# Performance work log

Measured on AMD Instinct MI355X. Metric: run time of the kernel, lower is better.

## Reference

```python
import jax, jax.numpy as jnp
import numpy as np

H = 256          # hidden_size
L = 2            # num_layers
K = 4            # khops
R = 128          # relation_num
N_NODES = 20000
N_EDGES = 160000
N_LG_EDGES = 640000


def setup_inputs() -> dict:
    key = jax.random.key(0)
    ks = iter(jax.random.split(key, 40))
    def nrm(shape, s=1.0):
        return jax.random.normal(next(ks), shape, dtype=jnp.float32) * s
    w = 1.0 / float(np.sqrt(H))
    return {
        "x": nrm((N_NODES, H)),
        "edge_feat": jax.random.randint(next(ks), (N_EDGES,), 0, R),
        "edge_index_g": jax.random.randint(next(ks), (2, N_EDGES), 0, N_NODES),
        "edge_index_lg": jax.random.randint(next(ks), (2, N_LG_EDGES), 0, N_EDGES),
        "rel_embed": nrm((R, H)),
        # per-layer, per-core (0=node update, 1=edge update) parameter stacks
        "w_self": nrm((L, 2, H, H), w), "b_self": jnp.zeros((L, 2, H), jnp.float32),
        "w_khop": nrm((L, 2, K, H, H), w), "b_khop": jnp.zeros((L, 2, K, H), jnp.float32),
        "w_fuse": nrm((L, 2, H, H), w), "b_fuse": jnp.zeros((L, 2, H), jnp.float32),
        "w_ff1": nrm((L, 2, H, 4 * H), w), "b_ff1": jnp.zeros((L, 2, 4 * H), jnp.float32),
        "w_ff2": nrm((L, 2, 4 * H, H), 1.0 / float(np.sqrt(4 * H))), "b_ff2": jnp.zeros((L, 2, H), jnp.float32),
        "ln1_g": jnp.ones((L, 2, H), jnp.float32), "ln1_b": jnp.zeros((L, 2, H), jnp.float32),
        "ln2_g": jnp.ones((L, 2, H), jnp.float32), "ln2_b": jnp.zeros((L, 2, H), jnp.float32),
    }


def _layernorm(x, g, b, eps=1e-5):
    m = jnp.mean(x, axis=-1, keepdims=True)
    v = jnp.var(x, axis=-1, keepdims=True)
    return (x - m) * jax.lax.rsqrt(v + eps) * g + b


def _core(p, src, dst, x, fused):
    """LGNNCore.forward (eval mode, dropout never applied in core)."""
    (ws, bs, wk, bk, wf, bf, w1, b1, w2, b2, g1, c1, g2, c2) = p
    n = x.shape[0]
    prev = x @ ws + bs
    # k-hop copy_src + sum aggregation, each hop gets its own linear
    z = x
    kh = jnp.zeros_like(prev)
    for i in range(wk.shape[0]):
        z = jax.ops.segment_sum(z[src], dst, num_segments=n)
        kh = kh + z @ wk[i] + bk[i]
    edge = fused @ wf + bf
    out = jax.nn.gelu(prev + kh + edge, approximate=False)
    out = _layernorm(x + out, g1, c1)
    ffn = jax.nn.gelu(out @ w1 + b1, approximate=False) @ w2 + b2
    return _layernorm(out + ffn, g2, c2)


def reference(x, edge_feat, edge_index_g, edge_index_lg, rel_embed,
              w_self, b_self, w_khop, b_khop, w_fuse, b_fuse,
              w_ff1, b_ff1, w_ff2, b_ff2, ln1_g, ln1_b, ln2_g, ln2_b):
    lg_x = rel_embed[edge_feat]                       # [n_edges, H]
    src_g, dst_g = edge_index_g[0], edge_index_g[1]
    src_l, dst_l = edge_index_lg[0], edge_index_lg[1]
    n_nodes = x.shape[0]
    for l in range(w_self.shape[0]):
        def pick(c):
            return (w_self[l, c], b_self[l, c], w_khop[l, c], b_khop[l, c],
                    w_fuse[l, c], b_fuse[l, c], w_ff1[l, c], b_ff1[l, c],
                    w_ff2[l, c], b_ff2[l, c], ln1_g[l, c], ln1_b[l, c],
                    ln2_g[l, c], ln2_b[l, c])
        # pmpd @ lg_x : scatter each edge feature to both of its endpoints
        fused_nodes = (jax.ops.segment_sum(lg_x, src_g, num_segments=n_nodes)
                       + jax.ops.segment_sum(lg_x, dst_g, num_segments=n_nodes))
        # pmpd^T @ x : gather both endpoint node features per edge
        fused_edges = x[src_g] + x[dst_g]
        new_x = _core(pick(0), src_g, dst_g, x, fused_nodes)
        new_lg_x = _core(pick(1), src_l, dst_l, lg_x, fused_edges)
        x, lg_x = new_x, new_lg_x
    return x, lg_x
```

## Files before the change

### kernel.cpp

```cpp
#include <hip/hip_runtime.h>

typedef __bf16 bf16;
typedef __attribute__((ext_vector_type(8))) __bf16 bf16x8;
typedef __attribute__((ext_vector_type(4))) __bf16 bf16x4;
typedef __attribute__((ext_vector_type(4))) float f32x4;

#define HD 256
#define GEMM_GELU 2

__device__ __forceinline__ float gelu_f(float x) {
  return 0.5f * x * (1.0f + erff(x * 0.70710678118654752440f));
}

__device__ __forceinline__ void gload_lds16(const void* g, void* l) {
  __builtin_amdgcn_global_load_lds(
      (const __attribute__((address_space(1))) unsigned int*)g,
      (__attribute__((address_space(3))) unsigned int*)l, 16, 0, 0);
}

__global__ __launch_bounds__(256) void gemm_k(
    const bf16* __restrict__ A, const bf16* __restrict__ Wt,
    const float* __restrict__ bias, bf16* __restrict__ C,
    int M, int Kd, int lda, int ldc, int flags)
{
  __shared__ __align__(16) bf16 sA[128 * 32];
  __shared__ __align__(16) bf16 sB[128 * 32];
  const int t = threadIdx.x;
  const int lane = t & 63, w = t >> 6;
  const int n0 = blockIdx.x * 128, m0 = blockIdx.y * 128;
  const int wr = w >> 1, wc = w & 1;
  const int lm = lane & 15, quad = lane >> 4;

  const int srow = t >> 2;
  const int scolb = (t & 3) * 16;
  const bool full = (m0 + 128 <= M);

  const char* a0 = (const char*)(A + (size_t)(m0 + srow) * lda) + scolb;
  const char* a1 = (const char*)(A + (size_t)(m0 + srow + 64) * lda) + scolb;
  const char* b0 = (const char*)(Wt + (size_t)(n0 + srow) * Kd) + scolb;
  const char* b1 = (const char*)(Wt + (size_t)(n0 + srow + 64) * Kd) + scolb;
  bf16* lA0 = sA + w * 512;
  bf16* lA1 = sA + 2048 + w * 512;
  bf16* lB0 = sB + w * 512;
  bf16* lB1 = sB + 2048 + w * 512;

  f32x4 acc[4][4];
#pragma unroll
  for (int i = 0; i < 4; i++)
#pragma unroll
    for (int j = 0; j < 4; j++)
#pragma unroll
      for (int r = 0; r < 4; r++) acc[i][j][r] = 0.f;

  for (int kb = 0; kb < Kd; kb += 32) {
    size_t ko = (size_t)kb * 2;
    if (full) {
      gload_lds16(a0 + ko, lA0);
      gload_lds16(a1 + ko, lA1);
    } else {
#pragma unroll
      for (int c = 0; c < 2; c++) {
        int row = srow + c * 64;
        int gr = m0 + row;
        bf16x8 va;
#pragma unroll
        for (int q = 0; q < 8; q++) va[q] = (bf16)0.f;
        if (gr < M) va = *(const bf16x8*)((const char*)(A + (size_t)gr * lda) + ko + scolb);
        *(bf16x8*)(sA + row * 32 + (scolb >> 1)) = va;
      }
    }
    gload_lds16(b0 + ko, lB0);
    gload_lds16(b1 + ko, lB1);
    __syncthreads();
    bf16x8 af[4], bv[4];
#pragma unroll
    for (int i = 0; i < 4; i++) af[i] = *(const bf16x8*)(sA + (wr * 64 + i * 16 + lm) * 32 + quad * 8);
#pragma unroll
    for (int j = 0; j < 4; j++) bv[j] = *(const bf16x8*)(sB + (wc * 64 + j * 16 + lm) * 32 + quad * 8);
#pragma unroll
    for (int i = 0; i < 4; i++)
#pragma unroll
      for (int j = 0; j < 4; j++)
        acc[i][j] = __builtin_amdgcn_mfma_f32_16x16x32_bf16(af[i], bv[j], acc[i][j], 0, 0, 0);
    __syncthreads();
  }
#pragma unroll
  for (int i = 0; i < 4; i++) {
#pragma unroll
    for (int r = 0; r < 4; r++) {
      int gr = m0 + wr * 64 + i * 16 + quad * 4 + r;
      if (gr < M) {
#pragma unroll
        for (int j = 0; j < 4; j++) {
          int gc = n0 + wc * 64 + j * 16 + lm;
          float v = acc[i][j][r] + bias[gc];
          if (flags & GEMM_GELU) v = gelu_f(v);
          C[(size_t)gr * ldc + gc] = (bf16)v;
        }
      }
    }
  }
}

__global__ __launch_bounds__(256) void segsum_k(
    const int* __restrict__ offs, const int* __restrict__ cols,
    const bf16* __restrict__ in, int ldin, bf16* __restrict__ out, int ldout, int nseg)
{
  int wid = threadIdx.x >> 6, lane = threadIdx.x & 63;
  int seg = blockIdx.x * 4 + wid;
  if (seg >= nseg) return;
  int b = offs[seg], e = offs[seg + 1];
  float a0 = 0.f, a1 = 0.f, a2 = 0.f, a3 = 0.f;
  for (int i = b; i < e; i++) {
    int c = cols[i];
    bf16x4 v = *(const bf16x4*)(in + (size_t)c * ldin + lane * 4);
    a0 += (float)v.x; a1 += (float)v.y; a2 += (float)v.z; a3 += (float)v.w;
  }
  bf16x4 o = {(bf16)a0, (bf16)a1, (bf16)a2, (bf16)a3};
  *(bf16x4*)(out + (size_t)seg * ldout + lane * 4) = o;
}

__global__ __launch_bounds__(256) void ln_k(
    const bf16* __restrict__ X, int ldx, const bf16* __restrict__ A,
    const float* __restrict__ gam, const float* __restrict__ bet,
    bf16* __restrict__ outb, float* __restrict__ outf, int M, int apply_gelu)
{
  int wid = threadIdx.x >> 6, lane = threadIdx.x & 63;
  int row = blockIdx.x * 4 + wid;
  if (row >= M) return;
  size_t xbase = (size_t)row * ldx + lane * 4;
  size_t abase = (size_t)row * HD + lane * 4;
  bf16x4 xv = *(const bf16x4*)(X + xbase);
  bf16x4 av = *(const bf16x4*)(A + abase);
  float s0, s1, s2, s3;
  if (apply_gelu) {
    s0 = (float)xv.x + gelu_f((float)av.x);
    s1 = (float)xv.y + gelu_f((float)av.y);
    s2 = (float)xv.z + gelu_f((float)av.z);
    s3 = (float)xv.w + gelu_f((float)av.w);
  } else {
    s0 = (float)xv.x + (float)av.x;
    s1 = (float)xv.y + (float)av.y;
    s2 = (float)xv.z + (float)av.z;
    s3 = (float)xv.w + (float)av.w;
  }
  float sum = s0 + s1 + s2 + s3;
#pragma unroll
  for (int o = 32; o; o >>= 1) sum += __shfl_xor(sum, o, 64);
  float mean = sum * (1.0f / 256.0f);
  float d0 = s0 - mean, d1 = s1 - mean, d2 = s2 - mean, d3 = s3 - mean;
  float vs = d0 * d0 + d1 * d1 + d2 * d2 + d3 * d3;
#pragma unroll
  for (int o = 32; o; o >>= 1) vs += __shfl_xor(vs, o, 64);
  float rstd = rsqrtf(vs * (1.0f / 256.0f) + 1e-5f);
  float4 g = *(const float4*)(gam + lane * 4);
  float4 bb = *(const float4*)(bet + lane * 4);
  float y0 = d0 * rstd * g.x + bb.x;
  float y1 = d1 * rstd * g.y + bb.y;
  float y2 = d2 * rstd * g.z + bb.z;
  float y3 = d3 * rstd * g.w + bb.w;
  if (outb) {
    bf16x4 o = {(bf16)y0, (bf16)y1, (bf16)y2, (bf16)y3};
    *(bf16x4*)(outb + xbase) = o;
  }
  if (outf) {
    float4 o = {y0, y1, y2, y3};
    *(float4*)(outf + abase) = o;
  }
}

__global__ __launch_bounds__(256) void gather_rel_k(
    const int* __restrict__ feat, const float* __restrict__ rel,
    bf16* __restrict__ out, int ldout, int NE)
{
  int wid = threadIdx.x >> 6, lane = threadIdx.x & 63;
  int e = blockIdx.x * 4 + wid;
  if (e >= NE) return;
  int f = feat[e];
  float4 v = *(const float4*)(rel + (size_t)f * HD + lane * 4);
  bf16x4 o = {(bf16)v.x, (bf16)v.y, (bf16)v.z, (bf16)v.w};
  *(bf16x4*)(out + (size_t)e * ldout + lane * 4) = o;
}

__global__ __launch_bounds__(256) void gather2_k(
    const int* __restrict__ src, const int* __restrict__ dst,
    const bf16* __restrict__ x, int ldx, bf16* __restrict__ out, int ldout, int NE)
{
  int wid = threadIdx.x >> 6, lane = threadIdx.x & 63;
  int e = blockIdx.x * 4 + wid;
  if (e >= NE) return;
  int s = src[e], d = dst[e];
  bf16x4 a = *(const bf16x4*)(x + (size_t)s * ldx + lane * 4);
  bf16x4 b = *(const bf16x4*)(x + (size_t)d * ldx + lane * 4);
  bf16x4 o = {(bf16)((float)a.x + (float)b.x), (bf16)((float)a.y + (float)b.y),
              (bf16)((float)a.z + (float)b.z), (bf16)((float)a.w + (float)b.w)};
  *(bf16x4*)(out + (size_t)e * ldout + lane * 4) = o;
}

__global__ __launch_bounds__(256) void f2b_k(const float* __restrict__ in,
                                             bf16* __restrict__ out, int ldout, int M) {
  int wid = threadIdx.x >> 6, lane = threadIdx.x & 63;
  int row = blockIdx.x * 4 + wid;
  if (row >= M) return;
  float4 v = *(const float4*)(in + (size_t)row * HD + lane * 4);
  bf16x4 o = {(bf16)v.x, (bf16)v.y, (bf16)v.z, (bf16)v.w};
  *(bf16x4*)(out + (size_t)row * ldout + lane * 4) = o;
}

__global__ __launch_bounds__(256) void wtrans_k(const float* __restrict__ in, bf16* __restrict__ out,
                                                int Kd, int Nd) {
  size_t moff = (size_t)blockIdx.y * Kd * Nd;
  int id = blockIdx.x * 256 + threadIdx.x;
  if (id >= Kd * Nd) return;
  int n = id / Kd, k = id - n * Kd;
  out[moff + id] = (bf16)in[moff + (size_t)k * Nd + n];
}

__global__ __launch_bounds__(256) void wcat_k(const float* __restrict__ ws, const float* __restrict__ wk,
                                              const float* __restrict__ wf, bf16* __restrict__ out,
                                              int KH, int CW) {
  int mi = blockIdx.y;
  int id = blockIdx.x * 256 + threadIdx.x;
  if (id >= HD * CW) return;
  int n = id / CW, k = id - n * CW;
  int s = k >> 8, kk = k & 255;
  float v;
  if (s == 0)       v = ws[((size_t)mi * HD + kk) * HD + n];
  else if (s <= KH) v = wk[(((size_t)mi * KH + (s - 1)) * HD + kk) * HD + n];
  else              v = wf[((size_t)mi * HD + kk) * HD + n];
  out[(size_t)mi * HD * CW + id] = (bf16)v;
}

__global__ __launch_bounds__(256) void bcat_k(const float* __restrict__ bs, const float* __restrict__ bk,
                                              const float* __restrict__ bf, float* __restrict__ out, int KH) {
  int mi = blockIdx.x, n = threadIdx.x;
  float v = bs[(size_t)mi * HD + n] + bf[(size_t)mi * HD + n];
  for (int i = 0; i < KH; i++) v += bk[((size_t)mi * KH + i) * HD + n];
  out[(size_t)mi * HD + n] = v;
}

__global__ __launch_bounds__(256) void count_k(const int* __restrict__ keys, int n, int* __restrict__ cnt) {
  int i = blockIdx.x * 256 + threadIdx.x;
  if (i < n) atomicAdd(&cnt[keys[i]], 1);
}
__global__ __launch_bounds__(256) void scan1_k(const int* __restrict__ in, int* __restrict__ out,
                                               int* __restrict__ bsum, int n) {
  __shared__ int sh[256];
  int t = threadIdx.x;
  int i0 = blockIdx.x * 1024 + t * 4;
  int v0 = (i0 < n) ? in[i0] : 0;
  int v1 = (i0 + 1 < n) ? in[i0 + 1] : 0;
  int v2 = (i0 + 2 < n) ? in[i0 + 2] : 0;
  int v3 = (i0 + 3 < n) ? in[i0 + 3] : 0;
  int tsum = v0 + v1 + v2 + v3;
  sh[t] = tsum;
  __syncthreads();
  for (int o = 1; o < 256; o <<= 1) {
    int x = (t >= o) ? sh[t - o] : 0;
    __syncthreads();
    sh[t] += x;
    __syncthreads();
  }
  int e0 = sh[t] - tsum;
  if (t == 255) bsum[blockIdx.x] = sh[255];
  if (i0 < n) out[i0] = e0;
  e0 += v0;
  if (i0 + 1 < n) out[i0 + 1] = e0;
  e0 += v1;
  if (i0 + 2 < n) out[i0 + 2] = e0;
  e0 += v2;
  if (i0 + 3 < n) out[i0 + 3] = e0;
}
__global__ void scan2_k(int* bsum, int nb, int* total) {
  if (threadIdx.x == 0 && blockIdx.x == 0) {
    int acc = 0;
    for (int i = 0; i < nb; i++) { int v = bsum[i]; bsum[i] = acc; acc += v; }
    *total = acc;
  }
}
__global__ __launch_bounds__(256) void scan3_k(int* out, const int* bsum, int n) {
  int i = blockIdx.x * 256 + threadIdx.x;
  if (i < n) out[i] += bsum[i >> 10];
}
__global__ __launch_bounds__(256) void fill_k(const int* __restrict__ keys, const int* __restrict__ vals,
                                              int n, int modE, int* __restrict__ cursor, int* __restrict__ cols) {
  int i = blockIdx.x * 256 + threadIdx.x;
  if (i >= n) return;
  int pos = atomicAdd(&cursor[keys[i]], 1);
  cols[pos] = vals ? vals[i] : (i < modE ? i : i - modE);
}

extern "C" void kernel_launch(void* const* d_in, const int* in_sizes, int n_in,
                              void* d_out, int out_size, void* d_ws, size_t ws_size,
                              hipStream_t stream)
{
  const float* x_in      = (const float*)d_in[0];
  const int*   edge_feat = (const int*)d_in[1];
  const int*   eig       = (const int*)d_in[2];
  const int*   eil       = (const int*)d_in[3];
  const float* rel       = (const float*)d_in[4];
  const float* w_self = (const float*)d_in[5];
  const float* b_self = (const float*)d_in[6];
  const float* w_khop = (const float*)d_in[7];
  const float* b_khop = (const float*)d_in[8];
  const float* w_fuse = (const float*)d_in[9];
  const float* b_fuse = (const float*)d_in[10];
  const float* w_ff1  = (const float*)d_in[11];
  const float* b_ff1  = (const float*)d_in[12];
  const float* w_ff2  = (const float*)d_in[13];
  const float* b_ff2  = (const float*)d_in[14];
  const float* ln1_g  = (const float*)d_in[15];
  const float* ln1_b  = (const float*)d_in[16];
  const float* ln2_g  = (const float*)d_in[17];
  const float* ln2_b  = (const float*)d_in[18];

  const int NN = in_sizes[0] / HD;
  const int NE = in_sizes[1];
  const int NL = in_sizes[3] / 2;
  const int L  = in_sizes[5] / (2 * HD * HD);
  const int KH = in_sizes[7] / (L * 2 * HD * HD);
  const int CW = (KH + 2) * HD;

  char* p = (char*)d_ws;
  auto alloc = [&](size_t bytes) -> void* {
    void* r = (void*)p;
    p += (bytes + 255) & ~(size_t)255;
    return r;
  };

  bf16* n_cat  = (bf16*)alloc((size_t)NN * CW * 2);
  bf16* lg_cat = (bf16*)alloc((size_t)NE * CW * 2);
  bf16* acc_n  = (bf16*)alloc((size_t)NN * HD * 2);
  bf16* acc_e  = (bf16*)alloc((size_t)NE * HD * 2);

  bf16*  wcat_t = (bf16*)alloc((size_t)L * 2 * HD * CW * 2);
  float* bcat   = (float*)alloc((size_t)L * 2 * HD * 4);
  bf16*  wff1_t = (bf16*)alloc((size_t)L * 2 * HD * 4 * HD * 2);
  bf16*  wff2_t = (bf16*)alloc((size_t)L * 2 * HD * 4 * HD * 2);

  int* inc_offs = (int*)alloc((size_t)(NN + 1) * 4);
  int* inc_cur  = (int*)alloc((size_t)NN * 4);
  int* inc_cols = (int*)alloc((size_t)2 * NE * 4);
  int* ng_offs  = (int*)alloc((size_t)(NN + 1) * 4);
  int* ng_cur   = (int*)alloc((size_t)NN * 4);
  int* ng_cols  = (int*)alloc((size_t)NE * 4);
  int* lg_offs  = (int*)alloc((size_t)(NE + 1) * 4);
  int* lg_cur   = (int*)alloc((size_t)NE * 4);
  int* lg_cols  = (int*)alloc((size_t)NL * 4);
  int* bsum     = (int*)alloc(3 * 256 * 4);

  wcat_k<<<dim3((HD * CW + 255) / 256, L * 2), 256, 0, stream>>>(w_self, w_khop, w_fuse, wcat_t, KH, CW);
  bcat_k<<<L * 2, 256, 0, stream>>>(b_self, b_khop, b_fuse, bcat, KH);
  wtrans_k<<<dim3((HD * 4 * HD + 255) / 256, L * 2), 256, 0, stream>>>(w_ff1, wff1_t, HD, 4 * HD);
  wtrans_k<<<dim3((HD * 4 * HD + 255) / 256, L * 2), 256, 0, stream>>>(w_ff2, wff2_t, 4 * HD, HD);

  f2b_k<<<(NN + 3) / 4, 256, 0, stream>>>(x_in, n_cat, CW, NN);
  gather_rel_k<<<(NE + 3) / 4, 256, 0, stream>>>(edge_feat, rel, lg_cat, CW, NE);

  auto build_csr = [&](const int* keys, int nkeys, const int* vals, int modE,
                       int nseg, int* offs, int* cur, int* cols, int* bs) {
    int nb = (nseg + 1023) / 1024;
    hipMemsetAsync(offs, 0, (size_t)(nseg + 1) * 4, stream);
    count_k<<<(nkeys + 255) / 256, 256, 0, stream>>>(keys, nkeys, offs);
    scan1_k<<<nb, 256, 0, stream>>>(offs, offs, bs, nseg);
    scan2_k<<<1, 1, 0, stream>>>(bs, nb, offs + nseg);
    scan3_k<<<(nseg + 255) / 256, 256, 0, stream>>>(offs, bs, nseg);
    hipMemcpyAsync(cur, offs, (size_t)nseg * 4, hipMemcpyDeviceToDevice, stream);
    fill_k<<<(nkeys + 255) / 256, 256, 0, stream>>>(keys, vals, nkeys, modE, cur, cols);
  };
  build_csr(eig, 2 * NE, nullptr, NE, NN, inc_offs, inc_cur, inc_cols, bsum);
  build_csr(eig + NE, NE, eig, 0, NN, ng_offs, ng_cur, ng_cols, bsum + 256);
  build_csr(eil + NL, NL, eil, 0, NE, lg_offs, lg_cur, lg_cols, bsum + 512);

  float* out_x  = (float*)d_out;
  float* out_lg = (float*)d_out + (size_t)NN * HD;

  auto run_core = [&](bf16* cat, bf16* accb, const int* coffs, const int* ccols,
                      int M, int l, int c, float* outf) {
    size_t mi = (size_t)(l * 2 + c);
    int mb = (M + 127) / 128;
    for (int i = 1; i <= KH; i++)
      segsum_k<<<(M + 3) / 4, 256, 0, stream>>>(coffs, ccols, cat + (size_t)(i - 1) * HD, CW,
                                                cat + (size_t)i * HD, CW, M);
    gemm_k<<<dim3(2, mb), 256, 0, stream>>>(cat, wcat_t + mi * HD * CW, bcat + mi * HD,
                                            accb, M, CW, CW, HD, 0);
    ln_k<<<(M + 3) / 4, 256, 0, stream>>>(cat, CW, accb, ln1_g + mi * HD, ln1_b + mi * HD,
                                          cat, (float*)nullptr, M, 1);
    gemm_k<<<dim3(8, mb), 256, 0, stream>>>(cat, wff1_t + mi * HD * 4 * HD, b_ff1 + mi * 4 * HD,
                                            cat + HD, M, HD, CW, CW, GEMM_GELU);
    gemm_k<<<dim3(2, mb), 256, 0, stream>>>(cat + HD, wff2_t + mi * 4 * HD * HD, b_ff2 + mi * HD,
                                            accb, M, 4 * HD, CW, HD, 0);
    ln_k<<<(M + 3) / 4, 256, 0, stream>>>(cat, CW, accb, ln2_g + mi * HD, ln2_b + mi * HD,
                                          cat, outf, M, 0);
  };

  for (int l = 0; l < L; l++) {
    segsum_k<<<(NN + 3) / 4, 256, 0, stream>>>(inc_offs, inc_cols, lg_cat, CW,
                                               n_cat + (size_t)(KH + 1) * HD, CW, NN);
    gather2_k<<<(NE + 3) / 4, 256, 0, stream>>>(eig, eig + NE, n_cat, CW,
                                                lg_cat + (size_t)(KH + 1) * HD, CW, NE);
    run_core(n_cat, acc_n, ng_offs, ng_cols, NN, l, 0, (l == L - 1) ? out_x : nullptr);
    run_core(lg_cat, acc_e, lg_offs, lg_cols, NE, l, 1, (l == L - 1) ? out_lg : nullptr);
  }
}
```

Measured before the change: 3.624 ms.

## Swizzle GEMM LDS, vectorize epilogue, tanh GELU, chunk FFN for cache reuse

Several changes land together. LDS tiles get an XOR swizzle to cut bank conflicts, and the MFMA operands are swapped so each lane holds four consecutive output columns, which allows vectorized bias loads and bf16x4 stores. The exact erf GELU is replaced by the tanh/sigmoid approximation using __expf. The FFN is also split into row chunks of 40000 that write the hidden activation to one reused buffer, so the intermediate can stay in cache. The GELU approximation changes numerics slightly, and the chunking adds more kernel launches for the edge graph.

```diff
diff --git a/kernel.cpp b/kernel.cpp
--- a/kernel.cpp
+++ b/kernel.cpp
@@ -9,7 +9,10 @@
 #define GEMM_GELU 2
 
 __device__ __forceinline__ float gelu_f(float x) {
-  return 0.5f * x * (1.0f + erff(x * 0.70710678118654752440f));
+  float x2 = x * x;
+  float u = 1.5957691216057308f * x * fmaf(0.044715f, x2, 1.0f);
+  float e = __expf(-u);
+  return x / (1.0f + e);
 }
 
 __device__ __forceinline__ void gload_lds16(const void* g, void* l) {
@@ -32,17 +35,19 @@
   const int lm = lane & 15, quad = lane >> 4;
 
   const int srow = t >> 2;
-  const int scolb = (t & 3) * 16;
+  const int cg = (t & 3) ^ ((t >> 3) & 3);
   const bool full = (m0 + 128 <= M);
 
-  const char* a0 = (const char*)(A + (size_t)(m0 + srow) * lda) + scolb;
-  const char* a1 = (const char*)(A + (size_t)(m0 + srow + 64) * lda) + scolb;
-  const char* b0 = (const char*)(Wt + (size_t)(n0 + srow) * Kd) + scolb;
-  const char* b1 = (const char*)(Wt + (size_t)(n0 + srow + 64) * Kd) + scolb;
+  const char* a0 = (const char*)(A + (size_t)(m0 + srow) * lda) + cg * 16;
+  const char* a1 = (const char*)(A + (size_t)(m0 + srow + 64) * lda) + cg * 16;
+  const char* b0 = (const char*)(Wt + (size_t)(n0 + srow) * Kd) + cg * 16;
+  const char* b1 = (const char*)(Wt + (size_t)(n0 + srow + 64) * Kd) + cg * 16;
   bf16* lA0 = sA + w * 512;
   bf16* lA1 = sA + 2048 + w * 512;
   bf16* lB0 = sB + w * 512;
   bf16* lB1 = sB + 2048 + w * 512;
+
+  const int soff = (quad ^ ((lm >> 1) & 3)) * 8;
 
   f32x4 acc[4][4];
 #pragma unroll
@@ -65,8 +70,8 @@
         bf16x8 va;
 #pragma unroll
         for (int q = 0; q < 8; q++) va[q] = (bf16)0.f;
-        if (gr < M) va = *(const bf16x8*)((const char*)(A + (size_t)gr * lda) + ko + scolb);
-        *(bf16x8*)(sA + row * 32 + (scolb >> 1)) = va;
+        if (gr < M) va = *(const bf16x8*)((const char*)(A + (size_t)gr * lda) + ko + cg * 16);
+        *(bf16x8*)(sA + row * 32 + (t & 3) * 8) = va;
       }
     }
     gload_lds16(b0 + ko, lB0);
@@ -74,29 +79,34 @@
     __syncthreads();
     bf16x8 af[4], bv[4];
 #pragma unroll
-    for (int i = 0; i < 4; i++) af[i] = *(const bf16x8*)(sA + (wr * 64 + i * 16 + lm) * 32 + quad * 8);
-#pragma unroll
-    for (int j = 0; j < 4; j++) bv[j] = *(const bf16x8*)(sB + (wc * 64 + j * 16 + lm) * 32 + quad * 8);
+    for (int i = 0; i < 4; i++) af[i] = *(const bf16x8*)(sA + (wr * 64 + i * 16 + lm) * 32 + soff);
+#pragma unroll
+    for (int j = 0; j < 4; j++) bv[j] = *(const bf16x8*)(sB + (wc * 64 + j * 16 + lm) * 32 + soff);
 #pragma unroll
     for (int i = 0; i < 4; i++)
 #pragma unroll
       for (int j = 0; j < 4; j++)
-        acc[i][j] = __builtin_amdgcn_mfma_f32_16x16x32_bf16(af[i], bv[j], acc[i][j], 0, 0, 0);
+        acc[i][j] = __builtin_amdgcn_mfma_f32_16x16x32_bf16(bv[j], af[i], acc[i][j], 0, 0, 0);
     __syncthreads();
   }
 #pragma unroll
   for (int i = 0; i < 4; i++) {
-#pragma unroll
-    for (int r = 0; r < 4; r++) {
-      int gr = m0 + wr * 64 + i * 16 + quad * 4 + r;
-      if (gr < M) {
-#pragma unroll
-        for (int j = 0; j < 4; j++) {
-          int gc = n0 + wc * 64 + j * 16 + lm;
-          float v = acc[i][j][r] + bias[gc];
-          if (flags & GEMM_GELU) v = gelu_f(v);
-          C[(size_t)gr * ldc + gc] = (bf16)v;
+    int gr = m0 + wr * 64 + i * 16 + lm;
+    if (gr < M) {
+      bf16* crow = C + (size_t)gr * ldc;
+#pragma unroll
+      for (int j = 0; j < 4; j++) {
+        int gc = n0 + wc * 64 + j * 16 + quad * 4;
+        float4 bia = *(const float4*)(bias + gc);
+        float v0 = acc[i][j][0] + bia.x;
+        float v1 = acc[i][j][1] + bia.y;
+        float v2 = acc[i][j][2] + bia.z;
+        float v3 = acc[i][j][3] + bia.w;
+        if (flags & GEMM_GELU) {
+          v0 = gelu_f(v0); v1 = gelu_f(v1); v2 = gelu_f(v2); v3 = gelu_f(v3);
         }
+        bf16x4 o = {(bf16)v0, (bf16)v1, (bf16)v2, (bf16)v3};
+        *(bf16x4*)(crow + gc) = o;
       }
     }
   }
@@ -386,10 +396,16 @@
                                             accb, M, CW, CW, HD, 0);
     ln_k<<<(M + 3) / 4, 256, 0, stream>>>(cat, CW, accb, ln1_g + mi * HD, ln1_b + mi * HD,
                                           cat, (float*)nullptr, M, 1);
-    gemm_k<<<dim3(8, mb), 256, 0, stream>>>(cat, wff1_t + mi * HD * 4 * HD, b_ff1 + mi * 4 * HD,
-                                            cat + HD, M, HD, CW, CW, GEMM_GELU);
-    gemm_k<<<dim3(2, mb), 256, 0, stream>>>(cat + HD, wff2_t + mi * 4 * HD * HD, b_ff2 + mi * HD,
-                                            accb, M, 4 * HD, CW, HD, 0);
+    bf16* hid = cat + HD;
+    int FC = (M > 40000) ? 40000 : M;
+    for (int c0 = 0; c0 < M; c0 += FC) {
+      int mc = (M - c0 < FC) ? (M - c0) : FC;
+      int mbc = (mc + 127) / 128;
+      gemm_k<<<dim3(8, mbc), 256, 0, stream>>>(cat + (size_t)c0 * CW, wff1_t + mi * HD * 4 * HD,
+                                               b_ff1 + mi * 4 * HD, hid, mc, HD, CW, CW, GEMM_GELU);
+      gemm_k<<<dim3(2, mbc), 256, 0, stream>>>(hid, wff2_t + mi * 4 * HD * HD, b_ff2 + mi * HD,
+                                               accb + (size_t)c0 * HD, mc, 4 * HD, CW, HD, 0);
+    }
     ln_k<<<(M + 3) / 4, 256, 0, stream>>>(cat, CW, accb, ln2_g + mi * HD, ln2_b + mi * HD,
                                           cat, outf, M, 0);
   };
```

Measured after the change: 3.332 ms. 8.0% less time.
